# Optimization experiments

Measured on AMD Instinct MI355X. Metric: run time of the kernel, lower is better.

Reference implementation:

```python
import jax, jax.numpy as jnp
import numpy as np

D_MODEL = 1024
N_HEADS = 16  # long-term branch; short/medium use N_HEADS // 2


def _band_bias(seq_len, scale_factor):
    # Intended semantics of create_temporal_mask: position i may attend to
    # positions j >= i - scale_factor (recent past + all future); positions
    # further than scale_factor in the past are blocked.
    i = jnp.arange(seq_len)[:, None]
    j = jnp.arange(seq_len)[None, :]
    return jnp.where(j >= i - scale_factor, 0.0, -1e9).astype(jnp.float32)


def _mha(x, w_in, b_in, w_out, b_out, n_heads, bias):
    # Faithful nn.MultiheadAttention (batch_first, eval/no dropout).
    B, S, D = x.shape
    dk = D // n_heads
    qkv = x @ w_in.T + b_in                       # [B,S,3D]
    q, k, v = jnp.split(qkv, 3, axis=-1)
    def heads(t):
        return t.reshape(B, S, n_heads, dk).transpose(0, 2, 1, 3)  # [B,H,S,dk]
    q, k, v = heads(q), heads(k), heads(v)
    scores = jnp.einsum('bhid,bhjd->bhij', q, k) / np.sqrt(dk).astype(np.float32)
    if bias is not None:
        scores = scores + bias
    attn = jax.nn.softmax(scores, axis=-1)        # [B,H,S,S]
    out = jnp.einsum('bhij,bhjd->bhid', attn, v)  # [B,H,S,dk]
    out = out.transpose(0, 2, 1, 3).reshape(B, S, D)
    return out @ w_out.T + b_out, attn


def _layernorm(x, gamma, beta, eps=1e-5):
    mu = jnp.mean(x, axis=-1, keepdims=True)
    var = jnp.var(x, axis=-1, keepdims=True)
    return (x - mu) * jax.lax.rsqrt(var + eps) * gamma + beta


def setup_inputs() -> dict:
    key = jax.random.key(0)
    ks = jax.random.split(key, 12)
    D = D_MODEL
    s = 0.02
    inp = {
        'x': jax.random.normal(ks[0], (2, 2048, D), dtype=jnp.float32),
        'w_in_s': jax.random.normal(ks[1], (3 * D, D), dtype=jnp.float32) * s,
        'b_in_s': jnp.zeros((3 * D,), dtype=jnp.float32),
        'wo_s': jax.random.normal(ks[2], (D, D), dtype=jnp.float32) * s,
        'bo_s': jnp.zeros((D,), dtype=jnp.float32),
        'w_in_m': jax.random.normal(ks[3], (3 * D, D), dtype=jnp.float32) * s,
        'b_in_m': jnp.zeros((3 * D,), dtype=jnp.float32),
        'wo_m': jax.random.normal(ks[4], (D, D), dtype=jnp.float32) * s,
        'bo_m': jnp.zeros((D,), dtype=jnp.float32),
        'w_in_l': jax.random.normal(ks[5], (3 * D, D), dtype=jnp.float32) * s,
        'b_in_l': jnp.zeros((3 * D,), dtype=jnp.float32),
        'wo_l': jax.random.normal(ks[6], (D, D), dtype=jnp.float32) * s,
        'bo_l': jnp.zeros((D,), dtype=jnp.float32),
        'w_comb': jax.random.normal(ks[7], (D, 3 * D), dtype=jnp.float32) * s,
        'b_comb': jnp.zeros((D,), dtype=jnp.float32),
        'gamma': jnp.ones((D,), dtype=jnp.float32),
        'beta': jnp.zeros((D,), dtype=jnp.float32),
    }
    return inp


def reference(x, w_in_s, b_in_s, wo_s, bo_s,
              w_in_m, b_in_m, wo_m, bo_m,
              w_in_l, b_in_l, wo_l, bo_l,
              w_comb, b_comb, gamma, beta):
    B, S, D = x.shape
    short_bias = _band_bias(S, 10)
    medium_bias = _band_bias(S, 30)
    short_out, _ = _mha(x, w_in_s, b_in_s, wo_s, bo_s, N_HEADS // 2, short_bias)
    medium_out, _ = _mha(x, w_in_m, b_in_m, wo_m, bo_m, N_HEADS // 2, medium_bias)
    long_out, attn = _mha(x, w_in_l, b_in_l, wo_l, bo_l, N_HEADS, None)
    attn_weights = jnp.mean(attn, axis=1)  # torch default average_attn_weights=True -> [B,S,S]
    combined = jnp.concatenate([short_out, medium_out, long_out], axis=-1)
    output = combined @ w_comb.T + b_comb
    return _layernorm(output + x, gamma, beta), attn_weights
```

## Files before the change

kernel.cpp:

```cpp
#include <hip/hip_runtime.h>
#include <hip/hip_bf16.h>
#include <math.h>

#define B_ 2
#define S_ 2048
#define D_ 1024
#define M_ (B_*S_)
#define CTXLD 3072

typedef _Float16 half8_t __attribute__((ext_vector_type(8)));
typedef _Float16 half4_t __attribute__((ext_vector_type(4)));
typedef float    f32x4  __attribute__((ext_vector_type(4)));

#define GL2LDS(g, l) __builtin_amdgcn_global_load_lds( \
    (const __attribute__((address_space(1))) void*)(uintptr_t)(g), \
    (__attribute__((address_space(3))) void*)(l), 16, 0, 0)

struct GemmBatch {
    const _Float16* A;
    const _Float16* W;
    const float*    bias;
    void*           C;
    void*           C2;
};

template<int MODE, int NB>
__global__ __launch_bounds__(256) void gemm_f16(
    GemmBatch b0, GemmBatch b1, GemmBatch b2, int lda, int ldw, int ldc, int K)
{
    constexpr int NT = NB / 32;
    __shared__ __align__(16) _Float16 As[2*128*32];
    __shared__ __align__(16) _Float16 Bs[2*NB*32];

    const GemmBatch G = (blockIdx.z == 0) ? b0 : ((blockIdx.z == 1) ? b1 : b2);

    const int t = threadIdx.x, lane = t & 63, w = t >> 6;
    const int bm = blockIdx.x * 128, bn = blockIdx.y * NB;
    const int wm = (w >> 1) * 64, wn = (w & 1) * (NB/2);
    const int fr = lane & 15, q8 = (lane >> 4) * 8;
    const int srow = lane >> 2, scol = (lane & 3) * 8;

    f32x4 acc[4][NT] = {};

    const _Float16* Ab = G.A + (size_t)(bm + w*32 + srow) * lda + scol;
    const _Float16* Wb = G.W + (size_t)(bn + w*(NB/4) + srow) * ldw + scol;

    for (int k0 = 0; k0 < K; k0 += 64) {
        __syncthreads();
        #pragma unroll
        for (int kc = 0; kc < 2; kc++) {
            #pragma unroll
            for (int ii = 0; ii < 2; ii++)
                GL2LDS(Ab + (size_t)(ii*16)*lda + k0 + kc*32,
                       As + kc*4096 + w*1024 + ii*512);
            #pragma unroll
            for (int ii = 0; ii < NB/64; ii++)
                GL2LDS(Wb + (size_t)(ii*16)*ldw + k0 + kc*32,
                       Bs + kc*NB*32 + w*(NB/4)*32 + ii*512);
        }
        __syncthreads();
        #pragma unroll
        for (int kc = 0; kc < 2; kc++) {
            half8_t af[4], bf[NT];
            #pragma unroll
            for (int mt = 0; mt < 4; mt++)
                af[mt] = *(const half8_t*)&As[kc*4096 + (wm + mt*16 + fr)*32 + q8];
            #pragma unroll
            for (int nt = 0; nt < NT; nt++)
                bf[nt] = *(const half8_t*)&Bs[kc*NB*32 + (wn + nt*16 + fr)*32 + q8];
            #pragma unroll
            for (int mt = 0; mt < 4; mt++)
                #pragma unroll
                for (int nt = 0; nt < NT; nt++)
                    acc[mt][nt] = __builtin_amdgcn_mfma_f32_16x16x32_f16(
                        af[mt], bf[nt], acc[mt][nt], 0, 0, 0);
        }
    }

    const int cl = lane & 15;
    const int rq = (lane >> 4) * 4;

    if (MODE == 2 && bn >= 2048) {
        #pragma unroll
        for (int mt = 0; mt < 4; mt++) {
            int row0 = bm + wm + mt*16 + rq;
            #pragma unroll
            for (int nt = 0; nt < NT; nt++) {
                int gcol = bn + wn + nt*16 + cl;
                float bv = G.bias[gcol];
                half4_t hv = {(_Float16)(acc[mt][nt][0] + bv),
                              (_Float16)(acc[mt][nt][1] + bv),
                              (_Float16)(acc[mt][nt][2] + bv),
                              (_Float16)(acc[mt][nt][3] + bv)};
                *(half4_t*)((_Float16*)G.C2 + (size_t)(gcol - 2048) * M_ + row0) = hv;
            }
        }
        return;
    }

    #pragma unroll
    for (int mt = 0; mt < 4; mt++) {
        #pragma unroll
        for (int r = 0; r < 4; r++) {
            size_t grow = (size_t)(bm + wm + mt*16 + rq + r);
            #pragma unroll
            for (int nt = 0; nt < NT; nt++) {
                int gcol = bn + wn + nt*16 + cl;
                float v = acc[mt][nt][r] + ((MODE == 3) ? 0.f : G.bias[gcol]);
                if (MODE == 0)
                    ((float*)G.C)[grow * ldc + gcol] = v;
                else
                    ((_Float16*)G.C)[grow * ldc + gcol] = (_Float16)v;
            }
        }
    }
}

struct CastArgs {
    const float* s[5];
    _Float16*    d[5];
    int          nb[5];
};

__global__ __launch_bounds__(256) void cast_all(CastArgs a)
{
    int off = blockIdx.x;
    int seg = 0;
    while (seg < 4 && off >= a.nb[seg]) { off -= a.nb[seg]; seg++; }
    int i = off * 256 + threadIdx.x;
    float4 v = ((const float4*)a.s[seg])[i];
    half4_t h = {(_Float16)v.x, (_Float16)v.y, (_Float16)v.z, (_Float16)v.w};
    ((half4_t*)a.d[seg])[i] = h;
}

__global__ __launch_bounds__(256) void transpose_cast_wo(
    const float* s0, const float* s1, const float* s2,
    _Float16* d0, _Float16* d1, _Float16* d2)
{
    __shared__ float T[64][68];
    const float* src = blockIdx.z == 0 ? s0 : (blockIdx.z == 1 ? s1 : s2);
    _Float16*    dst = blockIdx.z == 0 ? d0 : (blockIdx.z == 1 ? d1 : d2);
    const int db = blockIdx.x * 64;
    const int eb = blockIdx.y * 64;
    const int r = threadIdx.x >> 4;
    const int c = (threadIdx.x & 15) * 4;

    #pragma unroll
    for (int rr = 0; rr < 4; rr++) {
        float4 v = *(const float4*)&src[(size_t)(db + rr*16 + r)*1024 + eb + c];
        T[rr*16 + r][c+0] = v.x; T[rr*16 + r][c+1] = v.y;
        T[rr*16 + r][c+2] = v.z; T[rr*16 + r][c+3] = v.w;
    }
    __syncthreads();
    #pragma unroll
    for (int rr = 0; rr < 4; rr++) {
        int e = rr*16 + r;
        half4_t hv = {(_Float16)T[c+0][e], (_Float16)T[c+1][e],
                      (_Float16)T[c+2][e], (_Float16)T[c+3][e]};
        *(half4_t*)&dst[(size_t)(eb + e)*1024 + db + c] = hv;
    }
}

__global__ __launch_bounds__(256) void beff_kernel(
    const float* __restrict__ w_comb, const float* __restrict__ b_comb,
    const float* __restrict__ bo_s, const float* __restrict__ bo_m,
    const float* __restrict__ bo_l, float* __restrict__ beff)
{
    __shared__ float red[4];
    const int n = blockIdx.x, t = threadIdx.x;
    float s = 0.f;
    for (int d = t; d < 1024; d += 256)
        s += w_comb[(size_t)n*3072 + d]        * bo_s[d]
           + w_comb[(size_t)n*3072 + 1024 + d] * bo_m[d]
           + w_comb[(size_t)n*3072 + 2048 + d] * bo_l[d];
    #pragma unroll
    for (int m = 32; m >= 1; m >>= 1) s += __shfl_xor(s, m);
    if ((t & 63) == 0) red[t >> 6] = s;
    __syncthreads();
    if (t == 0) beff[n] = b_comb[n] + red[0] + red[1] + red[2] + red[3];
}

template<int DK, int BJ, bool LOUT>
__device__ __forceinline__ void flash_body(
    _Float16* lds, float* Lw,
    const _Float16* __restrict__ qk, const _Float16* __restrict__ vT,
    _Float16* __restrict__ ctx, float* __restrict__ lout,
    int window, int b, int h, int qblk, int H)
{
    constexpr int KS  = DK / 32;
    constexpr int DT  = DK / 16;
    constexpr int JT  = BJ / 16;
    constexpr int JC  = BJ / 32;
    constexpr int LDP = 40;

    _Float16* Ks = lds;
    _Float16* Vs = lds + DK*BJ;
    _Float16* Ps = lds + 2*DK*BJ;

    const int t = threadIdx.x, lane = t & 63, w = t >> 6;
    const int fr = lane & 15, g = lane >> 4, k8 = g * 8;
    const int k8s = (g ^ ((fr >> 1) & 3)) * 8;
    const int blkQ = qblk * 64;
    const int qlo  = blkQ + w * 16;

    const float sc = ((DK == 128) ? 0.08838834764831845f : 0.125f) * 1.44269504f;

    _Float16* PsW = Ps + w * 16 * LDP;
    const int srow = lane >> 2;
    const int ssw  = ((lane & 3) ^ ((srow >> 1) & 3)) * 8;

    half8_t qf[KS];
    #pragma unroll
    for (int kk = 0; kk < KS; kk++)
        qf[kk] = *(const half8_t*)&qk[(size_t)(b*S_ + qlo + fr)*2048 + h*DK + kk*32 + k8];

    f32x4 O[DT] = {};
    float lsum = 0.f;

    for (int j0 = 0; j0 < S_; j0 += BJ) {
        if (window >= 0 && j0 + BJ - 1 < blkQ - window) continue;
        __syncthreads();

        #pragma unroll
        for (int kk = 0; kk < KS; kk++)
            #pragma unroll
            for (int ii = 0; ii < BJ/64; ii++)
                GL2LDS(&qk[(size_t)(b*S_ + j0 + w*(BJ/4) + ii*16 + srow)*2048
                           + 1024 + h*DK + kk*32 + ssw],
                       &Ks[kk*BJ*32 + w*(BJ/4)*32 + ii*512]);
        #pragma unroll
        for (int jc = 0; jc < JC; jc++)
            #pragma unroll
            for (int ii = 0; ii < DK/64; ii++)
                GL2LDS(&vT[(size_t)(h*DK + w*(DK/4) + ii*16 + srow)*M_
                           + b*S_ + j0 + jc*32 + ssw],
                       &Vs[jc*DK*32 + w*(DK/4)*32 + ii*512]);
        __syncthreads();

        f32x4 st[JT];
        #pragma unroll
        for (int jt = 0; jt < JT; jt++) {
            f32x4 s = {};
            #pragma unroll
            for (int kk = 0; kk < KS; kk++) {
                half8_t kf = *(const half8_t*)&Ks[kk*BJ*32 + (jt*16 + fr)*32 + k8s];
                s = __builtin_amdgcn_mfma_f32_16x16x32_f16(kf, qf[kk], s, 0, 0, 0);
            }
            st[jt] = s;
        }

        const bool full = (window < 0) || (j0 >= qlo + 15 - window);
        #pragma unroll
        for (int kc = 0; kc < JC; kc++) {
            #pragma unroll
            for (int jh = 0; jh < 2; jh++) {
                int jt = kc*2 + jh;
                float p[4];
                #pragma unroll
                for (int r = 0; r < 4; r++) {
                    float pv = exp2f(st[jt][r] * sc);
                    if (!full) {
                        int jg = j0 + jt*16 + g*4 + r;
                        if (jg < (qlo + fr) - window) pv = 0.f;
                    }
                    p[r] = pv;
                    lsum += pv;
                }
                half4_t ph = {(_Float16)p[0], (_Float16)p[1],
                              (_Float16)p[2], (_Float16)p[3]};
                *(half4_t*)&PsW[fr*LDP + jh*16 + g*4] = ph;
            }
            half8_t pf = *(const half8_t*)&PsW[fr*LDP + k8];
            #pragma unroll
            for (int dt = 0; dt < DT; dt++) {
                half8_t vf = *(const half8_t*)&Vs[kc*DK*32 + (dt*16 + fr)*32 + k8s];
                O[dt] = __builtin_amdgcn_mfma_f32_16x16x32_f16(pf, vf, O[dt], 0, 0, 0);
            }
        }
    }

    lsum += __shfl_xor(lsum, 16);
    lsum += __shfl_xor(lsum, 32);
    if (g == 0) Lw[w*16 + fr] = lsum;
    float linv[4];
    #pragma unroll
    for (int r = 0; r < 4; r++)
        linv[r] = 1.f / Lw[w*16 + g*4 + r];

    if (LOUT && g == 0)
        lout[(size_t)(b*H + h)*S_ + qlo + fr] = lsum;

    #pragma unroll
    for (int r = 0; r < 4; r++) {
        _Float16* cp = ctx + (size_t)(b*S_ + qlo + g*4 + r)*CTXLD + h*DK;
        #pragma unroll
        for (int dt = 0; dt < DT; dt++)
            cp[dt*16 + fr] = (_Float16)(O[dt][r] * linv[r]);
    }
}

__global__ __launch_bounds__(256, 4) void flash_mega(
    const _Float16* __restrict__ qk_s, const _Float16* __restrict__ qk_m,
    const _Float16* __restrict__ qk_l,
    const _Float16* __restrict__ vT_s, const _Float16* __restrict__ vT_m,
    const _Float16* __restrict__ vT_l,
    _Float16* __restrict__ ctxall, float* __restrict__ lbuf)
{
    __shared__ __align__(16) _Float16 lds[18944];
    __shared__ float Lw[64];

    const int hwb = blockIdx.x;
    const int bid = (hwb & 7) * 256 + (hwb >> 3);
    if (bid < 1024) {
        int qblk = bid & 31, h = (bid >> 5) & 15, b = bid >> 9;
        flash_body<64, 128, true>(lds, Lw, qk_l, vT_l, ctxall + 2048, lbuf,
                                  -1, b, h, qblk, 16);
    } else {
        int r = bid - 1024;
        int qblk = r & 31;
        int h = (r >> 5) & 7;
        int z = r >> 8;
        int br = z >> 1, b = z & 1;
        flash_body<128, 64, false>(lds, Lw, br ? qk_m : qk_s, br ? vT_m : vT_s,
                                   ctxall + (br ? 1024 : 0), nullptr,
                                   br ? 30 : 10, b, h, qblk, 8);
    }
}

__global__ __launch_bounds__(256, 4) void attn_mean3(
    const _Float16* __restrict__ qk,
    const float* __restrict__ lbuf,
    float* __restrict__ attn)
{
    __shared__ __align__(16) _Float16 Ks[2 * 2 * 128 * 32];

    const int t = threadIdx.x, lane = t & 63, w = t >> 6;
    const int fr = lane & 15, g = lane >> 4, k8 = g * 8;
    const int k8s = (g ^ ((fr >> 1) & 3)) * 8;
    const int j0 = blockIdx.x * 128;
    const int irow = blockIdx.y * 64 + w * 16;
    const int b = blockIdx.z;
    const float c1 = 0.125f * 1.44269504f;
    const int srow = lane >> 2;
    const int ssw  = ((lane & 3) ^ ((srow >> 1) & 3)) * 8;

    f32x4 acc[8] = {};

    for (int hp = 0; hp < 16; hp += 2) {
        __syncthreads();
        #pragma unroll
        for (int hh = 0; hh < 2; hh++)
            #pragma unroll
            for (int kk = 0; kk < 2; kk++)
                #pragma unroll
                for (int ii = 0; ii < 2; ii++)
                    GL2LDS(&qk[(size_t)(b*S_ + j0 + w*32 + ii*16 + srow)*2048
                               + 1024 + (hp+hh)*64 + kk*32 + ssw],
                           &Ks[hh*8192 + kk*4096 + w*1024 + ii*512]);
        __syncthreads();

        #pragma unroll
        for (int hh = 0; hh < 2; hh++) {
            const int h = hp + hh;
            half8_t af[2];
            #pragma unroll
            for (int kk = 0; kk < 2; kk++)
                af[kk] = *(const half8_t*)
                    &qk[(size_t)(b*S_ + irow + fr)*2048 + h*64 + kk*32 + k8];

            float lg[4];
            #pragma unroll
            for (int r = 0; r < 4; r++)
                lg[r] = __log2f(lbuf[(size_t)(b*16 + h)*S_ + irow + g*4 + r]) + 4.0f;

            #pragma unroll
            for (int nt = 0; nt < 8; nt++) {
                f32x4 s = {};
                #pragma unroll
                for (int kk = 0; kk < 2; kk++) {
                    half8_t bf = *(const half8_t*)
                        &Ks[hh*8192 + kk*4096 + (nt*16 + fr)*32 + k8s];
                    s = __builtin_amdgcn_mfma_f32_16x16x32_f16(af[kk], bf, s, 0, 0, 0);
                }
                #pragma unroll
                for (int r = 0; r < 4; r++)
                    acc[nt][r] += exp2f(s[r] * c1 - lg[r]);
            }
        }
    }

    #pragma unroll
    for (int r = 0; r < 4; r++) {
        float* p = attn + (size_t)(b*S_ + irow + g*4 + r)*S_ + j0;
        #pragma unroll
        for (int nt = 0; nt < 8; nt++)
            p[nt*16 + fr] = acc[nt][r];
    }
}

__global__ __launch_bounds__(256) void ln_residual(
    const float* __restrict__ pre, const float* __restrict__ x,
    const float* __restrict__ gamma, const float* __restrict__ beta,
    float* __restrict__ out)
{
    __shared__ float redS[4], redQ[4];
    const int row = blockIdx.x;
    const int t = threadIdx.x;
    size_t base = (size_t)row * D_ + t * 4;

    float4 v  = *(const float4*)(pre + base);
    float4 xv = *(const float4*)(x + base);
    v.x += xv.x; v.y += xv.y; v.z += xv.z; v.w += xv.w;

    float s = v.x + v.y + v.z + v.w;
    float q = v.x*v.x + v.y*v.y + v.z*v.z + v.w*v.w;
    #pragma unroll
    for (int m = 32; m >= 1; m >>= 1) {
        s += __shfl_xor(s, m);
        q += __shfl_xor(q, m);
    }
    int wave = t >> 6;
    if ((t & 63) == 0) { redS[wave] = s; redQ[wave] = q; }
    __syncthreads();
    s = redS[0] + redS[1] + redS[2] + redS[3];
    q = redQ[0] + redQ[1] + redQ[2] + redQ[3];

    float mean = s * (1.f / D_);
    float var  = q * (1.f / D_) - mean * mean;
    float rstd = rsqrtf(var + 1e-5f);

    float4 g  = *(const float4*)(gamma + t * 4);
    float4 be = *(const float4*)(beta + t * 4);
    float4 o;
    o.x = (v.x - mean) * rstd * g.x + be.x;
    o.y = (v.y - mean) * rstd * g.y + be.y;
    o.z = (v.z - mean) * rstd * g.z + be.z;
    o.w = (v.w - mean) * rstd * g.w + be.w;
    *(float4*)(out + base) = o;
}

extern "C" void kernel_launch(void* const* d_in, const int* in_sizes, int n_in,
                              void* d_out, int out_size, void* d_ws, size_t ws_size,
                              hipStream_t stream)
{
    (void)in_sizes; (void)n_in; (void)out_size; (void)ws_size;
    const float* x      = (const float*)d_in[0];
    const float* w_in_s = (const float*)d_in[1];
    const float* b_in_s = (const float*)d_in[2];
    const float* wo_s   = (const float*)d_in[3];
    const float* bo_s   = (const float*)d_in[4];
    const float* w_in_m = (const float*)d_in[5];
    const float* b_in_m = (const float*)d_in[6];
    const float* wo_m   = (const float*)d_in[7];
    const float* bo_m   = (const float*)d_in[8];
    const float* w_in_l = (const float*)d_in[9];
    const float* b_in_l = (const float*)d_in[10];
    const float* wo_l   = (const float*)d_in[11];
    const float* bo_l   = (const float*)d_in[12];
    const float* w_comb = (const float*)d_in[13];
    const float* b_comb = (const float*)d_in[14];
    const float* gamma  = (const float*)d_in[15];
    const float* beta   = (const float*)d_in[16];

    float* out    = (float*)d_out;
    float* attn_o = out + (size_t)M_ * D_;

    char* W = (char*)d_ws;
    _Float16* w_in_s_h = (_Float16*)(W);
    _Float16* w_in_m_h = (_Float16*)(W + 6291456);
    _Float16* w_in_l_h = (_Float16*)(W + 12582912);
    _Float16* w_comb_h = (_Float16*)(W + 18874368);
    _Float16* woT_s    = (_Float16*)(W + 25165824);
    _Float16* woT_m    = (_Float16*)(W + 27262976);
    _Float16* woT_l    = (_Float16*)(W + 29360128);
    _Float16* weff     = (_Float16*)(W + 31457280);
    _Float16* qk_s     = (_Float16*)(W + 37748736);
    _Float16* qk_m     = (_Float16*)(W + 54525952);
    _Float16* qk_l     = (_Float16*)(W + 71303168);
    _Float16* vT_s     = (_Float16*)(W + 88080384);
    _Float16* vT_m     = (_Float16*)(W + 96468992);
    _Float16* ctxall   = (_Float16*)(W + 104857600);
    _Float16* x_h      = (_Float16*)(W + 130023424);
    float*    lbuf     = (float*)   (W + 138412032);
    float*    beff     = (float*)   (W + 138674432);
    _Float16* vT_l     = w_comb_h;
    float*    pre      = (float*)qk_m;

    dim3 blk(256);
    GemmBatch nil = { nullptr, nullptr, nullptr, nullptr, nullptr };

    CastArgs ca;
    ca.s[0]=x;      ca.d[0]=x_h;      ca.nb[0]=4096;
    ca.s[1]=w_in_s; ca.d[1]=w_in_s_h; ca.nb[1]=3072;
    ca.s[2]=w_in_m; ca.d[2]=w_in_m_h; ca.nb[2]=3072;
    ca.s[3]=w_in_l; ca.d[3]=w_in_l_h; ca.nb[3]=3072;
    ca.s[4]=w_comb; ca.d[4]=w_comb_h; ca.nb[4]=3072;
    cast_all<<<dim3(16384), blk, 0, stream>>>(ca);

    transpose_cast_wo<<<dim3(16, 16, 3), blk, 0, stream>>>(
        wo_s, wo_m, wo_l, woT_s, woT_m, woT_l);

    GemmBatch we0 = { w_comb_h + 0,    woT_s, nullptr, weff + 0,    nullptr };
    GemmBatch we1 = { w_comb_h + 1024, woT_m, nullptr, weff + 1024, nullptr };
    GemmBatch we2 = { w_comb_h + 2048, woT_l, nullptr, weff + 2048, nullptr };
    gemm_f16<3, 64><<<dim3(8, 16, 3), blk, 0, stream>>>(we0, we1, we2, 3072, 1024, 3072, 1024);

    beff_kernel<<<dim3(1024), blk, 0, stream>>>(w_comb, b_comb, bo_s, bo_m, bo_l, beff);

    GemmBatch qs = { x_h, w_in_s_h, b_in_s, qk_s, vT_s };
    GemmBatch qm = { x_h, w_in_m_h, b_in_m, qk_m, vT_m };
    GemmBatch ql = { x_h, w_in_l_h, b_in_l, qk_l, vT_l };
    gemm_f16<2, 128><<<dim3(M_/128, 3072/128, 3), blk, 0, stream>>>(qs, qm, ql, D_, D_, 2048, D_);

    flash_mega<<<dim3(2048), blk, 0, stream>>>(
        qk_s, qk_m, qk_l, vT_s, vT_m, vT_l, ctxall, lbuf);

    attn_mean3<<<dim3(S_/128, S_/64, B_), blk, 0, stream>>>(qk_l, lbuf, attn_o);

    GemmBatch fb = { ctxall, weff, beff, pre, nullptr };
    gemm_f16<0, 64><<<dim3(M_/128, 1024/64, 1), blk, 0, stream>>>(fb, nil, nil, 3072, 3072, D_, 3072);

    ln_residual<<<dim3(M_), blk, 0, stream>>>(pre, x, gamma, beta, out);
}
```

Measured before the change: 538.4 us.

## Use 128-row query blocks with 512-thread flash CTAs and prescale Q in GEMM epilogue

```diff
diff --git a/kernel.cpp b/kernel.cpp
--- a/kernel.cpp
+++ b/kernel.cpp
@@ -15,6 +15,9 @@
 #define GL2LDS(g, l) __builtin_amdgcn_global_load_lds( \
     (const __attribute__((address_space(1))) void*)(uintptr_t)(g), \
     (__attribute__((address_space(3))) void*)(l), 16, 0, 0)
+
+#define QSC_L  0.18033688011112f
+#define QSC_SM 0.12751744707f
 
 struct GemmBatch {
     const _Float16* A;
@@ -98,6 +101,9 @@
         return;
     }
 
+    const float qsc = (MODE == 2 && bn < 1024)
+                      ? ((blockIdx.z == 2) ? QSC_L : QSC_SM) : 1.0f;
+
     #pragma unroll
     for (int mt = 0; mt < 4; mt++) {
         #pragma unroll
@@ -107,6 +113,7 @@
             for (int nt = 0; nt < NT; nt++) {
                 int gcol = bn + wn + nt*16 + cl;
                 float v = acc[mt][nt][r] + ((MODE == 3) ? 0.f : G.bias[gcol]);
+                if (MODE == 2) v *= qsc;
                 if (MODE == 0)
                     ((float*)G.C)[grow * ldc + gcol] = v;
                 else
@@ -192,6 +199,8 @@
     constexpr int JT  = BJ / 16;
     constexpr int JC  = BJ / 32;
     constexpr int LDP = 40;
+    constexpr int KRB = BJ / 16;
+    constexpr int VRB = DK / 16;
 
     _Float16* Ks = lds;
     _Float16* Vs = lds + DK*BJ;
@@ -200,10 +209,8 @@
     const int t = threadIdx.x, lane = t & 63, w = t >> 6;
     const int fr = lane & 15, g = lane >> 4, k8 = g * 8;
     const int k8s = (g ^ ((fr >> 1) & 3)) * 8;
-    const int blkQ = qblk * 64;
+    const int blkQ = qblk * 128;
     const int qlo  = blkQ + w * 16;
-
-    const float sc = ((DK == 128) ? 0.08838834764831845f : 0.125f) * 1.44269504f;
 
     _Float16* PsW = Ps + w * 16 * LDP;
     const int srow = lane >> 2;
@@ -222,19 +229,21 @@
         __syncthreads();
 
         #pragma unroll
-        for (int kk = 0; kk < KS; kk++)
-            #pragma unroll
-            for (int ii = 0; ii < BJ/64; ii++)
-                GL2LDS(&qk[(size_t)(b*S_ + j0 + w*(BJ/4) + ii*16 + srow)*2048
-                           + 1024 + h*DK + kk*32 + ssw],
-                       &Ks[kk*BJ*32 + w*(BJ/4)*32 + ii*512]);
-        #pragma unroll
-        for (int jc = 0; jc < JC; jc++)
-            #pragma unroll
-            for (int ii = 0; ii < DK/64; ii++)
-                GL2LDS(&vT[(size_t)(h*DK + w*(DK/4) + ii*16 + srow)*M_
-                           + b*S_ + j0 + jc*32 + ssw],
-                       &Vs[jc*DK*32 + w*(DK/4)*32 + ii*512]);
+        for (int i = 0; i < 2; i++) {
+            int u = w*2 + i;
+            int kk = u / KRB, rb = u % KRB;
+            GL2LDS(&qk[(size_t)(b*S_ + j0 + rb*16 + srow)*2048
+                       + 1024 + h*DK + kk*32 + ssw],
+                   &Ks[kk*BJ*32 + rb*512]);
+        }
+        #pragma unroll
+        for (int i = 0; i < 2; i++) {
+            int u = w*2 + i;
+            int jc = u / VRB, rb = u % VRB;
+            GL2LDS(&vT[(size_t)(h*DK + rb*16 + srow)*M_
+                       + b*S_ + j0 + jc*32 + ssw],
+                   &Vs[jc*DK*32 + rb*512]);
+        }
         __syncthreads();
 
         f32x4 st[JT];
@@ -258,7 +267,7 @@
                 float p[4];
                 #pragma unroll
                 for (int r = 0; r < 4; r++) {
-                    float pv = exp2f(st[jt][r] * sc);
+                    float pv = exp2f(st[jt][r]);
                     if (!full) {
                         int jg = j0 + jt*16 + g*4 + r;
                         if (jg < (qlo + fr) - window) pv = 0.f;
@@ -299,31 +308,31 @@
     }
 }
 
-__global__ __launch_bounds__(256, 4) void flash_mega(
+__global__ __launch_bounds__(512, 6) void flash_mega(
     const _Float16* __restrict__ qk_s, const _Float16* __restrict__ qk_m,
     const _Float16* __restrict__ qk_l,
     const _Float16* __restrict__ vT_s, const _Float16* __restrict__ vT_m,
     const _Float16* __restrict__ vT_l,
     _Float16* __restrict__ ctxall, float* __restrict__ lbuf)
 {
-    __shared__ __align__(16) _Float16 lds[18944];
-    __shared__ float Lw[64];
+    __shared__ __align__(16) _Float16 lds[21504];
+    __shared__ float Lw[128];
 
     const int hwb = blockIdx.x;
-    const int bid = (hwb & 7) * 256 + (hwb >> 3);
-    if (bid < 1024) {
-        int qblk = bid & 31, h = (bid >> 5) & 15, b = bid >> 9;
+    const int bid = (hwb & 7) * 128 + (hwb >> 3);
+    const int grp = bid >> 4, q = bid & 15;
+    if (!(grp & 1)) {
+        int lg = grp >> 1;
+        int b = lg >> 4, h = lg & 15;
         flash_body<64, 128, true>(lds, Lw, qk_l, vT_l, ctxall + 2048, lbuf,
-                                  -1, b, h, qblk, 16);
+                                  -1, b, h, q, 16);
     } else {
-        int r = bid - 1024;
-        int qblk = r & 31;
-        int h = (r >> 5) & 7;
-        int z = r >> 8;
-        int br = z >> 1, b = z & 1;
+        int sg = grp >> 1;
+        int z = sg >> 3;
+        int br = z >> 1, b = z & 1, h = sg & 7;
         flash_body<128, 64, false>(lds, Lw, br ? qk_m : qk_s, br ? vT_m : vT_s,
                                    ctxall + (br ? 1024 : 0), nullptr,
-                                   br ? 30 : 10, b, h, qblk, 8);
+                                   br ? 30 : 10, b, h, q, 8);
     }
 }
 
@@ -340,7 +349,6 @@
     const int j0 = blockIdx.x * 128;
     const int irow = blockIdx.y * 64 + w * 16;
     const int b = blockIdx.z;
-    const float c1 = 0.125f * 1.44269504f;
     const int srow = lane >> 2;
     const int ssw  = ((lane & 3) ^ ((srow >> 1) & 3)) * 8;
 
@@ -384,7 +392,7 @@
                 }
                 #pragma unroll
                 for (int r = 0; r < 4; r++)
-                    acc[nt][r] += exp2f(s[r] * c1 - lg[r]);
+                    acc[nt][r] += exp2f(s[r] - lg[r]);
             }
         }
     }
@@ -512,7 +520,7 @@
     GemmBatch ql = { x_h, w_in_l_h, b_in_l, qk_l, vT_l };
     gemm_f16<2, 128><<<dim3(M_/128, 3072/128, 3), blk, 0, stream>>>(qs, qm, ql, D_, D_, 2048, D_);
 
-    flash_mega<<<dim3(2048), blk, 0, stream>>>(
+    flash_mega<<<dim3(1024), dim3(512), 0, stream>>>(
         qk_s, qk_m, qk_l, vT_s, vT_m, vT_l, ctxall, lbuf);
 
     attn_mean3<<<dim3(S_/128, S_/64, B_), blk, 0, stream>>>(qk_l, lbuf, attn_o);
```

Result: slower. 636.6 us (+18.2%).
